# Performance work log

Hardware: AMD Instinct MI355X
Metric: run time of the kernel (lower is better)

The kernel has to match this reference:

```python
import jax, jax.numpy as jnp
import numpy as np

N = 20000      # nodes per snapshot
E = 160000     # edges per snapshot
T = 8          # timesteps
F_IN = 256     # nfeat
HEADS = 4      # GAT heads
C = 128        # nhid_graph (per-head GAT out, concat=False -> mean)
GH = 128       # nhid_gru
NC = 2         # nclass
NEG_SLOPE = 0.2


def setup_inputs() -> dict:
    key = jax.random.key(0)
    ks = jax.random.split(key, 16)
    s = 0.05
    return {
        "graph": jax.random.randint(ks[0], (T, 2, E), 0, N),
        "fts": jax.random.normal(ks[1], (T, N, F_IN), dtype=jnp.float32),
        "time_steps": T,
        # GATConv params (PyG-style): lin weight, att_src/att_dst, bias
        "W_gat": jax.random.normal(ks[2], (F_IN, HEADS * C), dtype=jnp.float32) * s,
        "att_src": jax.random.normal(ks[3], (HEADS, C), dtype=jnp.float32) * s,
        "att_dst": jax.random.normal(ks[4], (HEADS, C), dtype=jnp.float32) * s,
        "b_gat": jax.random.normal(ks[5], (C,), dtype=jnp.float32) * s,
        # GRU params (torch layout: [3H, in], gates order r,z,n)
        "W_ih": jax.random.normal(ks[6], (3 * GH, C), dtype=jnp.float32) * s,
        "W_hh": jax.random.normal(ks[7], (3 * GH, GH), dtype=jnp.float32) * s,
        "b_ih": jax.random.normal(ks[8], (3 * GH,), dtype=jnp.float32) * s,
        "b_hh": jax.random.normal(ks[9], (3 * GH,), dtype=jnp.float32) * s,
        # Attention ('general'): linear_in [H,H] no bias, linear_out [H,2H] no bias
        "W_att_in": jax.random.normal(ks[10], (GH, GH), dtype=jnp.float32) * s,
        "W_att_out": jax.random.normal(ks[11], (GH, 2 * GH), dtype=jnp.float32) * s,
        # final classifier
        "W_cls": jax.random.normal(ks[12], (NC, GH), dtype=jnp.float32) * s,
        "b_cls": jax.random.normal(ks[13], (NC,), dtype=jnp.float32) * s,
    }


def _segment_softmax(logits, seg, num_segments):
    # logits: [E', H], seg: [E'] destination node ids
    m = jax.ops.segment_max(logits, seg, num_segments=num_segments)
    m = jnp.where(jnp.isfinite(m), m, 0.0)
    e = jnp.exp(logits - m[seg])
    s = jax.ops.segment_sum(e, seg, num_segments=num_segments)
    return e / (s[seg] + 1e-16)


def _gat_step(x, edge_index, W_gat, att_src, att_dst, b_gat):
    # PyG GATConv: concat=False (mean over heads), negative_slope=0.2,
    # add_self_loops=True; eval mode so attention dropout is identity.
    n = x.shape[0]
    xw = (x @ W_gat).reshape(n, HEADS, C)                 # [N,H,C]
    loops = jnp.arange(n, dtype=edge_index.dtype)
    src = jnp.concatenate([edge_index[0], loops])         # [E']
    dst = jnp.concatenate([edge_index[1], loops])
    a_src = jnp.einsum('nhc,hc->nh', xw, att_src)         # [N,H]
    a_dst = jnp.einsum('nhc,hc->nh', xw, att_dst)
    alpha = jax.nn.leaky_relu(a_src[src] + a_dst[dst], NEG_SLOPE)  # [E',H]
    alpha = _segment_softmax(alpha, dst, n)
    msg = xw[src] * alpha[..., None]                      # [E',H,C]
    out = jax.ops.segment_sum(msg, dst, num_segments=n)   # [N,H,C]
    return out.mean(axis=1) + b_gat                       # [N,C]


def _gru(y, W_ih, W_hh, b_ih, b_hh):
    # y: [T, N, C]; torch GRU equations, h0 = 0
    n = y.shape[1]
    def step(h, x):
        gi = x @ W_ih.T + b_ih
        gh = h @ W_hh.T + b_hh
        i_r, i_z, i_n = jnp.split(gi, 3, axis=-1)
        h_r, h_z, h_n = jnp.split(gh, 3, axis=-1)
        r = jax.nn.sigmoid(i_r + h_r)
        z = jax.nn.sigmoid(i_z + h_z)
        nn_ = jnp.tanh(i_n + r * h_n)
        h_new = (1.0 - z) * nn_ + z * h
        return h_new, h_new
    h0 = jnp.zeros((n, GH), dtype=y.dtype)
    last, full = jax.lax.scan(step, h0, y)
    return full, last  # [T,N,GH], [N,GH]


def reference(graph, fts, time_steps, W_gat, att_src, att_dst, b_gat,
              W_ih, W_hh, b_ih, b_hh, W_att_in, W_att_out, W_cls, b_cls):
    # per-timestep GAT + leaky_relu(0.2)
    ys = [jax.nn.leaky_relu(
            _gat_step(fts[i], graph[i], W_gat, att_src, att_dst, b_gat),
            NEG_SLOPE)
          for i in range(time_steps)]
    y = jnp.stack(ys)                                     # [T,N,C]
    context, last = _gru(y, W_ih, W_hh, b_ih, b_hh)
    query = last[:, None, :]                              # [N,1,GH]
    context = jnp.transpose(context, (1, 0, 2))           # [N,T,GH]
    # Attention('general')
    q = query @ W_att_in.T                                # [N,1,GH]
    scores = jnp.einsum('nod,ntd->not', q, context)       # [N,1,T]
    w = jax.nn.softmax(scores, axis=-1)
    mix = jnp.einsum('not,ntd->nod', w, context)          # [N,1,GH]
    combined = jnp.concatenate([mix, q], axis=-1)         # [N,1,2GH]
    att_out = jnp.tanh(combined @ W_att_out.T)            # [N,1,GH]
    output = jax.nn.leaky_relu(att_out.reshape(-1, GH), NEG_SLOPE)
    logits = output @ W_cls.T + b_cls                     # [N,NC]
    return jax.nn.log_softmax(logits, axis=1)
```

## Files before the change

### kernel.cpp

```cpp
#include <hip/hip_runtime.h>
#include <hip/hip_bf16.h>
#include <math.h>

#define N_NODES 20000
#define N_EDGES 160000
#define T_STEPS 8
#define F_INC   256
#define HEADS   4
#define CCH     128
#define KC      512
#define GHD     128
#define G3      384
#define SLOPE   0.2f
#define SEG     (N_EDGES + N_NODES)

typedef unsigned short u16;
typedef __attribute__((ext_vector_type(8))) short bf16x8;
typedef __attribute__((ext_vector_type(4))) float f32x4;

__device__ __forceinline__ float leakyf(float x) { return x > 0.f ? x : SLOPE * x; }
__device__ __forceinline__ float b2f(u16 u) {
  union { unsigned int i; float f; } x; x.i = ((unsigned int)u) << 16; return x.f;
}
__device__ __forceinline__ u16 f2b(float f) {
  union { float f; unsigned int i; } u; u.f = f;
  unsigned int r = u.i + 0x7FFFu + ((u.i >> 16) & 1u);
  return (u16)(r >> 16);
}
__device__ __forceinline__ float sigf(float x) { return 1.f / (1.f + expf(-x)); }

__device__ __forceinline__ void gload16(const void* g, void* l) {
  __builtin_amdgcn_global_load_lds(
      (const __attribute__((address_space(1))) unsigned int*)g,
      (__attribute__((address_space(3))) unsigned int*)l, 16, 0, 0);
}

__device__ __forceinline__ bf16x8 cvt8(f32x4 lo, f32x4 hi) {
  union { unsigned int u[4]; bf16x8 v; } r;
  asm("v_cvt_pk_bf16_f32 %0, %1, %2" : "=v"(r.u[0]) : "v"(lo[0]), "v"(lo[1]));
  asm("v_cvt_pk_bf16_f32 %0, %1, %2" : "=v"(r.u[1]) : "v"(lo[2]), "v"(lo[3]));
  asm("v_cvt_pk_bf16_f32 %0, %1, %2" : "=v"(r.u[2]) : "v"(hi[0]), "v"(hi[1]));
  asm("v_cvt_pk_bf16_f32 %0, %1, %2" : "=v"(r.u[3]) : "v"(hi[2]), "v"(hi[3]));
  return r.v;
}

template <int OBF, int FUSE, int AFP32>
__global__ __launch_bounds__(256) void gemm_bf16(
    const void* __restrict__ Ain, const u16* __restrict__ B,
    const float* __restrict__ bias, void* __restrict__ Cout,
    int M, int K, int Nt, int swz,
    const float* __restrict__ attS, const float* __restrict__ attD,
    float* __restrict__ asrc, float* __restrict__ adst)
{
  __shared__ __align__(16) char AsRaw[128 * 32 * 4];
  __shared__ u16 Bs[128][32];
  __shared__ float s_as[128], s_ad[128];
  float* AsF = (float*)AsRaw;
  u16 (*Asb)[32] = (u16(*)[32])AsRaw;
  const int tid  = threadIdx.x;
  const int wave = tid >> 6, lane = tid & 63;
  const int wr = (wave >> 1) * 64, wc = (wave & 1) * 64;
  int bx = blockIdx.x, by = blockIdx.y;
  if (swz) {
    const int gx = gridDim.x;
    const int nwg = gx * (int)gridDim.y;
    const int lin = by * gx + bx;
    const int q = nwg >> 3, r = nwg & 7;
    const int xcd = lin & 7, idx = lin >> 3;
    const int wg = (xcd < r ? xcd * (q + 1) : r * (q + 1) + (xcd - r) * q) + idx;
    bx = wg % gx; by = wg / gx;
  }
  const int bm = by * 128, bn = bx * 128;
  const int l15 = lane & 15, g = lane >> 4;

  if (FUSE && tid < 128) { s_as[tid] = 0.f; s_ad[tid] = 0.f; }

  const int sr = tid >> 2, sd = tid & 3;
  const int ss = sd ^ ((sr >> 1) & 3);
  const u16* aS0 = 0; const u16* aS1 = 0; u16* lA0 = 0; u16* lA1 = 0;
  const float* aF[4]; float* lAF[4];
  if (AFP32) {
    const float* Af = (const float*)Ain;
    const int row0 = tid >> 3, sd8 = tid & 7;
    const int ss8 = sd8 ^ (row0 & 7);
    #pragma unroll
    for (int p = 0; p < 4; ++p) {
      int row = row0 + p * 32;
      aF[p] = Af + (size_t)min(bm + row, M - 1) * K + ss8 * 4;
      lAF[p] = AsF + (size_t)(p * 256 + (tid & ~63)) * 4;
    }
  } else {
    const u16* Ab = (const u16*)Ain;
    aS0 = Ab + (size_t)min(bm + sr,      M - 1) * K + ss * 8;
    aS1 = Ab + (size_t)min(bm + 64 + sr, M - 1) * K + ss * 8;
    lA0 = (u16*)AsRaw + (size_t)(tid & ~63) * 8;
    lA1 = lA0 + 2048;
  }
  const u16* bS0 = B + (size_t)(bn + sr)      * K + ss * 8;
  const u16* bS1 = B + (size_t)(bn + 64 + sr) * K + ss * 8;
  u16* lB0 = &Bs[0][0] + (size_t)(tid & ~63) * 8;
  u16* lB1 = lB0 + 2048;

  f32x4 acc[4][4];
  #pragma unroll
  for (int m = 0; m < 4; ++m)
    #pragma unroll
    for (int n = 0; n < 4; ++n)
      #pragma unroll
      for (int j = 0; j < 4; ++j) acc[m][n][j] = 0.f;

  const int nK = K >> 5;
  for (int kt = 0; kt < nK; ++kt) {
    const int ko = kt * 32;
    if (AFP32) {
      #pragma unroll
      for (int p = 0; p < 4; ++p) gload16(aF[p] + ko, lAF[p]);
    } else {
      gload16(aS0 + ko, lA0);
      gload16(aS1 + ko, lA1);
    }
    gload16(bS0 + ko, lB0);
    gload16(bS1 + ko, lB1);
    __syncthreads();
    bf16x8 af[4], bfr[4];
    #pragma unroll
    for (int m = 0; m < 4; ++m) {
      int row = wr + m * 16 + l15;
      if (AFP32) {
        int s0 = (2 * g) ^ (row & 7), s1 = (2 * g + 1) ^ (row & 7);
        f32x4 lo = *(const f32x4*)&AsF[row * 32 + s0 * 4];
        f32x4 hi = *(const f32x4*)&AsF[row * 32 + s1 * 4];
        af[m] = cvt8(lo, hi);
      } else {
        af[m] = *(const bf16x8*)&Asb[row][(g ^ ((row >> 1) & 3)) * 8];
      }
      int rowb = wc + m * 16 + l15;
      bfr[m] = *(const bf16x8*)&Bs[rowb][(g ^ ((rowb >> 1) & 3)) * 8];
    }
    #pragma unroll
    for (int m = 0; m < 4; ++m)
      #pragma unroll
      for (int n = 0; n < 4; ++n)
        acc[m][n] = __builtin_amdgcn_mfma_f32_16x16x32_bf16(af[m], bfr[n], acc[m][n], 0, 0, 0);
    __syncthreads();
  }
  #pragma unroll
  for (int m = 0; m < 4; ++m) {
    int row0 = bm + wr + m * 16 + g * 4;
    #pragma unroll
    for (int n = 0; n < 4; ++n) {
      int col = bn + wc + n * 16 + l15;
      float bv = bias ? bias[col] : 0.f;
      #pragma unroll
      for (int j = 0; j < 4; ++j) {
        int row = row0 + j;
        if (row < M) {
          float v = acc[m][n][j] + bv;
          if (OBF) ((u16*)Cout)[(size_t)row * Nt + col] = f2b(v);
          else     ((float*)Cout)[(size_t)row * Nt + col] = v;
        }
      }
    }
  }
  if (FUSE) {
    float ps[4][4], pd[4][4];
    #pragma unroll
    for (int m = 0; m < 4; ++m)
      #pragma unroll
      for (int j = 0; j < 4; ++j) { ps[m][j] = 0.f; pd[m][j] = 0.f; }
    #pragma unroll
    for (int n = 0; n < 4; ++n) {
      int cl = wc + n * 16 + l15;
      float wsv = attS[bn + cl], wdv = attD[bn + cl];
      #pragma unroll
      for (int m = 0; m < 4; ++m)
        #pragma unroll
        for (int j = 0; j < 4; ++j) {
          ps[m][j] = fmaf(acc[m][n][j], wsv, ps[m][j]);
          pd[m][j] = fmaf(acc[m][n][j], wdv, pd[m][j]);
        }
    }
    #pragma unroll
    for (int m = 0; m < 4; ++m)
      #pragma unroll
      for (int j = 0; j < 4; ++j)
        #pragma unroll
        for (int msk = 8; msk >= 1; msk >>= 1) {
          ps[m][j] += __shfl_xor(ps[m][j], msk);
          pd[m][j] += __shfl_xor(pd[m][j], msk);
        }
    if (l15 == 0) {
      #pragma unroll
      for (int m = 0; m < 4; ++m)
        #pragma unroll
        for (int j = 0; j < 4; ++j) {
          atomicAdd(&s_as[wr + m * 16 + g * 4 + j], ps[m][j]);
          atomicAdd(&s_ad[wr + m * 16 + g * 4 + j], pd[m][j]);
        }
    }
    __syncthreads();
    if (tid < 128) {
      int row = bm + tid;
      if (row < M) {
        int h = bn >> 7;
        asrc[(size_t)row * 4 + h] = s_as[tid];
        adst[(size_t)row * 4 + h] = s_ad[tid];
      }
    }
  }
}

__global__ void convert_weights(const float* __restrict__ w_ih, const float* __restrict__ w_hh,
                                const float* __restrict__ w_in, const float* __restrict__ w_out,
                                u16* __restrict__ wihb, u16* __restrict__ whhb,
                                u16* __restrict__ winb, u16* __restrict__ woutb)
{
  int i = blockIdx.x * 256 + threadIdx.x;
  const float* src; u16* dst; int base;
  if      (i < 6144)  { src = w_ih;  dst = wihb;  base = i; }
  else if (i < 12288) { src = w_hh;  dst = whhb;  base = i - 6144; }
  else if (i < 14336) { src = w_in;  dst = winb;  base = i - 12288; }
  else                { src = w_out; dst = woutb; base = i - 14336; }
  int o = base * 8;
  float4 v0 = *(const float4*)(src + o);
  float4 v1 = *(const float4*)(src + o + 4);
  bf16x8 ov;
  ov[0] = (short)f2b(v0.x); ov[1] = (short)f2b(v0.y);
  ov[2] = (short)f2b(v0.z); ov[3] = (short)f2b(v0.w);
  ov[4] = (short)f2b(v1.x); ov[5] = (short)f2b(v1.y);
  ov[6] = (short)f2b(v1.z); ov[7] = (short)f2b(v1.w);
  *(bf16x8*)(dst + o) = ov;
}

__global__ void conv_transpose_wgat(const float* __restrict__ src, u16* __restrict__ dst) {
  int idx = blockIdx.x * 256 + threadIdx.x;
  if (idx >= KC * F_INC) return;
  int n = idx >> 8, k = idx & 255;
  dst[(size_t)n * F_INC + k] = f2b(src[(size_t)k * KC + n]);
}

__global__ void count_kernel(const int* __restrict__ graph, int* __restrict__ counts) {
  int e = blockIdx.x * 256 + threadIdx.x;
  int t = blockIdx.y;
  if (e < N_EDGES) {
    int d = graph[(size_t)t * 2 * N_EDGES + N_EDGES + e];
    atomicAdd(&counts[t * N_NODES + d], 1);
  }
}

__global__ __launch_bounds__(1024) void scan_kernel(
    const int* __restrict__ counts, int* __restrict__ offs)
{
  const int t = blockIdx.x;
  const int tid = threadIdx.x, lane = tid & 63, w = tid >> 6;
  __shared__ int s_wt[16];
  int carry = 0;
  const int base_abs = t * SEG;
  for (int base = 0; base < N_NODES; base += 1024) {
    int i = base + tid;
    int v = (i < N_NODES) ? (counts[t * N_NODES + i] + 1) : 0;
    int x = v;
    #pragma unroll
    for (int d = 1; d < 64; d <<= 1) {
      int nvl = __shfl_up(x, d, 64);
      if (lane >= d) x += nvl;
    }
    if (lane == 63) s_wt[w] = x;
    __syncthreads();
    if (tid < 16) {
      int y = s_wt[tid];
      #pragma unroll
      for (int d = 1; d < 16; d <<= 1) {
        int nvl = __shfl_up(y, d, 64);
        if (tid >= d) y += nvl;
      }
      s_wt[tid] = y;
    }
    __syncthreads();
    int wbase = (w > 0) ? s_wt[w - 1] : 0;
    int total = s_wt[15];
    if (i < N_NODES) offs[t * (N_NODES + 1) + i] = base_abs + carry + wbase + x - v;
    carry += total;
    __syncthreads();
  }
  if (tid == 0) offs[t * (N_NODES + 1) + N_NODES] = base_abs + carry;
}

__global__ void scatter_kernel(const int* __restrict__ graph, const int* __restrict__ offs,
                               int* __restrict__ cursor, int* __restrict__ ssrc)
{
  int i = blockIdx.x * 256 + threadIdx.x;
  int t = blockIdx.y;
  if (i >= SEG) return;
  int s, d;
  if (i < N_EDGES) {
    s = graph[(size_t)t * 2 * N_EDGES + i];
    d = graph[(size_t)t * 2 * N_EDGES + N_EDGES + i];
  } else {
    s = d = i - N_EDGES;
  }
  int pos = offs[t * (N_NODES + 1) + d] + atomicAdd(&cursor[t * N_NODES + d], 1);
  ssrc[pos] = s;
}

__global__ __launch_bounds__(256) void aggregate_kernel(
    const u16* __restrict__ xw, const float* __restrict__ a_src,
    const float* __restrict__ a_dst, const float* __restrict__ b_gat,
    const int* __restrict__ offs, const int* __restrict__ ssrc,
    u16* __restrict__ yout)
{
  const int wv = threadIdx.x >> 6, lane = threadIdx.x & 63;
  const int nd = blockIdx.x * 4 + wv;
  const int t  = blockIdx.y;
  const int ob = t * (N_NODES + 1) + nd;
  const int beg = offs[ob], end = offs[ob + 1];
  const size_t rowbase = (size_t)t * N_NODES;
  const int he   = lane & 3;
  const int eidx = lane >> 2;
  const int hl   = lane >> 4;
  const float advh = a_dst[(rowbase + nd) * 4 + he];

  float m = -INFINITY, ssum = 0.f;
  float acc[8] = {0.f,0.f,0.f,0.f,0.f,0.f,0.f,0.f};

#define FMA8(W, X)                                                        \
    { float _w = (W);                                                     \
      acc[0] = fmaf(_w, __uint_as_float((unsigned)(X).x << 16), acc[0]);  \
      acc[1] = fmaf(_w, __uint_as_float((unsigned)(X).x & 0xffff0000u), acc[1]); \
      acc[2] = fmaf(_w, __uint_as_float((unsigned)(X).y << 16), acc[2]);  \
      acc[3] = fmaf(_w, __uint_as_float((unsigned)(X).y & 0xffff0000u), acc[3]); \
      acc[4] = fmaf(_w, __uint_as_float((unsigned)(X).z << 16), acc[4]);  \
      acc[5] = fmaf(_w, __uint_as_float((unsigned)(X).z & 0xffff0000u), acc[5]); \
      acc[6] = fmaf(_w, __uint_as_float((unsigned)(X).w << 16), acc[6]);  \
      acc[7] = fmaf(_w, __uint_as_float((unsigned)(X).w & 0xffff0000u), acc[7]); }
#define LDE(SVAR) (*(const int4*)&xw[(rowbase + (SVAR)) * KC + lane * 8])

  for (int base = beg; base < end; base += 16) {
    const int cnt = min(16, end - base);
    const int e = base + eidx;
    const int sidx = (e < end) ? ssrc[e] : ssrc[base];
    const float av = a_src[(rowbase + sidx) * 4 + he];
    const float a = (eidx < cnt) ? leakyf(av + advh) : -INFINITY;
    float cm = a;
    cm = fmaxf(cm, __shfl_xor(cm, 4));
    cm = fmaxf(cm, __shfl_xor(cm, 8));
    cm = fmaxf(cm, __shfl_xor(cm, 16));
    cm = fmaxf(cm, __shfl_xor(cm, 32));
    const float nm = fmaxf(m, cm);
    const float sc = expf(m - nm);
    const float w = expf(a - nm);
    float ts = w;
    ts += __shfl_xor(ts, 4);
    ts += __shfl_xor(ts, 8);
    ts += __shfl_xor(ts, 16);
    ts += __shfl_xor(ts, 32);
    ssum = ssum * sc + ts;
    m = nm;
    const float schl = __shfl(sc, hl);
    #pragma unroll
    for (int k = 0; k < 8; ++k) acc[k] *= schl;

    const int cpad = (cnt + 3) & ~3;
    int b4 = 0;
    for (; b4 + 8 <= cpad; b4 += 8) {
      const int s0 = __shfl(sidx, (b4 + 0) << 2);
      const int s1 = __shfl(sidx, (b4 + 1) << 2);
      const int s2 = __shfl(sidx, (b4 + 2) << 2);
      const int s3 = __shfl(sidx, (b4 + 3) << 2);
      const int s4 = __shfl(sidx, (b4 + 4) << 2);
      const int s5 = __shfl(sidx, (b4 + 5) << 2);
      const int s6 = __shfl(sidx, (b4 + 6) << 2);
      const int s7 = __shfl(sidx, (b4 + 7) << 2);
      const int4 x0 = LDE(s0); const int4 x1 = LDE(s1);
      const int4 x2 = LDE(s2); const int4 x3 = LDE(s3);
      const int4 x4 = LDE(s4); const int4 x5 = LDE(s5);
      const int4 x6 = LDE(s6); const int4 x7 = LDE(s7);
      const float w0 = __shfl(w, ((b4 + 0) << 2) + hl);
      const float w1 = __shfl(w, ((b4 + 1) << 2) + hl);
      const float w2 = __shfl(w, ((b4 + 2) << 2) + hl);
      const float w3 = __shfl(w, ((b4 + 3) << 2) + hl);
      const float w4 = __shfl(w, ((b4 + 4) << 2) + hl);
      const float w5 = __shfl(w, ((b4 + 5) << 2) + hl);
      const float w6 = __shfl(w, ((b4 + 6) << 2) + hl);
      const float w7 = __shfl(w, ((b4 + 7) << 2) + hl);
      FMA8(w0, x0); FMA8(w1, x1); FMA8(w2, x2); FMA8(w3, x3);
      FMA8(w4, x4); FMA8(w5, x5); FMA8(w6, x6); FMA8(w7, x7);
    }
    if (b4 < cpad) {
      const int s0 = __shfl(sidx, (b4 + 0) << 2);
      const int s1 = __shfl(sidx, (b4 + 1) << 2);
      const int s2 = __shfl(sidx, (b4 + 2) << 2);
      const int s3 = __shfl(sidx, (b4 + 3) << 2);
      const int4 x0 = LDE(s0); const int4 x1 = LDE(s1);
      const int4 x2 = LDE(s2); const int4 x3 = LDE(s3);
      const float w0 = __shfl(w, ((b4 + 0) << 2) + hl);
      const float w1 = __shfl(w, ((b4 + 1) << 2) + hl);
      const float w2 = __shfl(w, ((b4 + 2) << 2) + hl);
      const float w3 = __shfl(w, ((b4 + 3) << 2) + hl);
      FMA8(w0, x0); FMA8(w1, x1); FMA8(w2, x2); FMA8(w3, x3);
    }
  }
#undef LDE
#undef FMA8

  const float sh = __shfl(ssum, hl);
  const float inv = 1.f / (sh + 1e-16f);
  #pragma unroll
  for (int k = 0; k < 8; ++k) {
    acc[k] *= inv;
    acc[k] += __shfl_xor(acc[k], 16);
    acc[k] += __shfl_xor(acc[k], 32);
  }
  if (lane < 16) {
    bf16x8 ov;
    #pragma unroll
    for (int k = 0; k < 8; ++k) {
      float v = acc[k] * 0.25f + b_gat[lane * 8 + k];
      ov[k] = (short)f2b(leakyf(v));
    }
    *(bf16x8*)&yout[(rowbase + nd) * GHD + lane * 8] = ov;
  }
}

__global__ __launch_bounds__(256) void gru_seq(
    const u16* __restrict__ Whh, const float* __restrict__ b_hh,
    const u16* __restrict__ giall, u16* __restrict__ ctx)
{
  __shared__ u16 hA[32][128];
  __shared__ u16 reg2[12288];
  u16 (*Bs)[32] = (u16(*)[32])reg2;
  const int tid = threadIdx.x, lane = tid & 63, wv = tid >> 6;
  const int l15 = lane & 15, g = lane >> 4;
  const int bm = blockIdx.x * 32;

  const int sr = tid >> 2, sd = tid & 3;
  const int ssb = sd ^ ((sr >> 1) & 3);
  const u16* bS[6]; u16* lB[6];
  #pragma unroll
  for (int p = 0; p < 6; ++p) {
    bS[p] = Whh + (size_t)(sr + p * 64) * GHD + ssb * 8;
    lB[p] = reg2 + (size_t)(p * 256 + (tid & ~63)) * 8;
  }
  float bbv[6];
  #pragma unroll
  for (int n = 0; n < 6; ++n) bbv[n] = b_hh[wv * 96 + n * 16 + l15];

  const int cr = tid >> 3;
  const int cg = (tid & 7) * 8;
  const int grow = bm + cr;
  const size_t gb = (size_t)grow * G3;
  const size_t cb = (size_t)grow * GHD;
  float hp[2][8];

  #pragma unroll
  for (int q = 0; q < 2; ++q) {
    const int c0 = cg + q * 64;
    bf16x8 ir8 = *(const bf16x8*)&giall[gb + c0];
    bf16x8 iz8 = *(const bf16x8*)&giall[gb + 128 + c0];
    bf16x8 in8 = *(const bf16x8*)&giall[gb + 256 + c0];
    float4 br0 = *(const float4*)&b_hh[c0];       float4 br1 = *(const float4*)&b_hh[c0 + 4];
    float4 bz0 = *(const float4*)&b_hh[128 + c0]; float4 bz1 = *(const float4*)&b_hh[128 + c0 + 4];
    float4 bn0 = *(const float4*)&b_hh[256 + c0]; float4 bn1 = *(const float4*)&b_hh[256 + c0 + 4];
    float bhr[8] = {br0.x, br0.y, br0.z, br0.w, br1.x, br1.y, br1.z, br1.w};
    float bhz[8] = {bz0.x, bz0.y, bz0.z, bz0.w, bz1.x, bz1.y, bz1.z, bz1.w};
    float bhn[8] = {bn0.x, bn0.y, bn0.z, bn0.w, bn1.x, bn1.y, bn1.z, bn1.w};
    bf16x8 hv;
    #pragma unroll
    for (int k = 0; k < 8; ++k) {
      float rr = sigf(b2f((u16)ir8[k]) + bhr[k]);
      float zz = sigf(b2f((u16)iz8[k]) + bhz[k]);
      float nn = tanhf(b2f((u16)in8[k]) + rr * bhn[k]);
      float h = (1.f - zz) * nn;
      hp[q][k] = h;
      hv[k] = (short)f2b(h);
    }
    const int sl = (c0 >> 3) ^ (cr & 7);
    *(bf16x8*)&hA[cr][sl * 8] = hv;
    *(bf16x8*)&ctx[cb + c0] = hv;
  }
  __syncthreads();

  for (int t = 1; t < T_STEPS; ++t) {
    const u16* gi_t = giall + (size_t)t * N_NODES * G3;
    u16* ctx_t = ctx + (size_t)t * N_NODES * GHD;
    f32x4 acc[2][6];
    #pragma unroll
    for (int m = 0; m < 2; ++m)
      #pragma unroll
      for (int n = 0; n < 6; ++n)
        #pragma unroll
        for (int j = 0; j < 4; ++j) acc[m][n][j] = 0.f;

    #pragma unroll
    for (int kt = 0; kt < 4; ++kt) {
      const int ko = kt * 32;
      #pragma unroll
      for (int p = 0; p < 6; ++p) gload16(bS[p] + ko, lB[p]);
      __syncthreads();
      bf16x8 af[2], bfr[6];
      #pragma unroll
      for (int m = 0; m < 2; ++m) {
        int row = m * 16 + l15;
        int sl = (kt * 4 + g) ^ (row & 7);
        af[m] = *(const bf16x8*)&hA[row][sl * 8];
      }
      #pragma unroll
      for (int n = 0; n < 6; ++n) {
        int rowb = wv * 96 + n * 16 + l15;
        bfr[n] = *(const bf16x8*)&Bs[rowb][(g ^ ((rowb >> 1) & 3)) * 8];
      }
      #pragma unroll
      for (int m = 0; m < 2; ++m)
        #pragma unroll
        for (int n = 0; n < 6; ++n)
          acc[m][n] = __builtin_amdgcn_mfma_f32_16x16x32_bf16(af[m], bfr[n], acc[m][n], 0, 0, 0);
      __syncthreads();
    }
    #pragma unroll
    for (int m = 0; m < 2; ++m)
      #pragma unroll
      for (int n = 0; n < 6; ++n) {
        int c = wv * 96 + n * 16 + l15;
        #pragma unroll
        for (int j = 0; j < 4; ++j) {
          int r = m * 16 + g * 4 + j;
          reg2[r * 384 + (((c >> 3) ^ (r & 7)) << 3) + (c & 7)] = f2b(acc[m][n][j] + bbv[n]);
        }
      }
    __syncthreads();
    #pragma unroll
    for (int q = 0; q < 2; ++q) {
      const int c0 = cg + q * 64;
      const int sl0 = ((c0 >> 3) ^ (cr & 7));
      const int sl1 = (((128 + c0) >> 3) ^ (cr & 7));
      const int sl2 = (((256 + c0) >> 3) ^ (cr & 7));
      bf16x8 hr8 = *(bf16x8*)&reg2[cr * 384 + sl0 * 8];
      bf16x8 hz8 = *(bf16x8*)&reg2[cr * 384 + sl1 * 8];
      bf16x8 hn8 = *(bf16x8*)&reg2[cr * 384 + sl2 * 8];
      bf16x8 ir8 = *(const bf16x8*)&gi_t[gb + c0];
      bf16x8 iz8 = *(const bf16x8*)&gi_t[gb + 128 + c0];
      bf16x8 in8 = *(const bf16x8*)&gi_t[gb + 256 + c0];
      bf16x8 hv;
      #pragma unroll
      for (int k = 0; k < 8; ++k) {
        float rr = sigf(b2f((u16)ir8[k]) + b2f((u16)hr8[k]));
        float zz = sigf(b2f((u16)iz8[k]) + b2f((u16)hz8[k]));
        float nn = tanhf(b2f((u16)in8[k]) + rr * b2f((u16)hn8[k]));
        float h = (1.f - zz) * nn + zz * hp[q][k];
        hp[q][k] = h;
        hv[k] = (short)f2b(h);
      }
      const int slh = (c0 >> 3) ^ (cr & 7);
      *(bf16x8*)&hA[cr][slh * 8] = hv;
      *(bf16x8*)&ctx_t[cb + c0] = hv;
    }
    __syncthreads();
  }
}

__global__ __launch_bounds__(256) void attn_mid(
    const u16* __restrict__ ctx, const float* __restrict__ q,
    u16* __restrict__ comb)
{
  const int node = blockIdx.x * 4 + (threadIdx.x >> 6);
  const int lane = threadIdx.x & 63;
  if (node >= N_NODES) return;
  const float q0 = q[(size_t)node * GHD + lane];
  const float q1 = q[(size_t)node * GHD + 64 + lane];
  float c0[T_STEPS], c1[T_STEPS], w[T_STEPS];
  float mx = -1e30f;
  #pragma unroll
  for (int t = 0; t < T_STEPS; ++t) {
    const u16* cr = ctx + ((size_t)t * N_NODES + node) * GHD;
    c0[t] = b2f(cr[lane]); c1[t] = b2f(cr[64 + lane]);
    float p = q0 * c0[t] + q1 * c1[t];
    #pragma unroll
    for (int m = 32; m >= 1; m >>= 1) p += __shfl_xor(p, m);
    w[t] = p;
    mx = fmaxf(mx, p);
  }
  float s = 0.f;
  #pragma unroll
  for (int t = 0; t < T_STEPS; ++t) { w[t] = expf(w[t] - mx); s += w[t]; }
  const float inv = 1.f / s;
  float m0 = 0.f, m1 = 0.f;
  #pragma unroll
  for (int t = 0; t < T_STEPS; ++t) { m0 = fmaf(w[t], c0[t], m0); m1 = fmaf(w[t], c1[t], m1); }
  m0 *= inv; m1 *= inv;
  u16* cb = comb + (size_t)node * 2 * GHD;
  cb[lane]       = f2b(m0);
  cb[64 + lane]  = f2b(m1);
  cb[128 + lane] = f2b(q0);
  cb[192 + lane] = f2b(q1);
}

__global__ __launch_bounds__(256) void logits_kernel(
    const u16* __restrict__ ao, const float* __restrict__ W_cls,
    const float* __restrict__ b_cls, float* __restrict__ out)
{
  const int node = blockIdx.x * 4 + (threadIdx.x >> 6);
  const int lane = threadIdx.x & 63;
  if (node >= N_NODES) return;
  float o0 = leakyf(tanhf(b2f(ao[(size_t)node * GHD + lane])));
  float o1 = leakyf(tanhf(b2f(ao[(size_t)node * GHD + 64 + lane])));
  float p0 = o0 * W_cls[lane] + o1 * W_cls[64 + lane];
  float p1 = o0 * W_cls[128 + lane] + o1 * W_cls[192 + lane];
  #pragma unroll
  for (int m = 32; m >= 1; m >>= 1) { p0 += __shfl_xor(p0, m); p1 += __shfl_xor(p1, m); }
  if (lane == 0) {
    float l0 = p0 + b_cls[0];
    float l1 = p1 + b_cls[1];
    float mx = fmaxf(l0, l1);
    float lse = mx + logf(expf(l0 - mx) + expf(l1 - mx));
    out[(size_t)node * 2 + 0] = l0 - lse;
    out[(size_t)node * 2 + 1] = l1 - lse;
  }
}

extern "C" void kernel_launch(void* const* d_in, const int* in_sizes, int n_in,
                              void* d_out, int out_size, void* d_ws, size_t ws_size,
                              hipStream_t stream)
{
  const int*   graph     = (const int*)  d_in[0];
  const float* fts       = (const float*)d_in[1];
  const float* W_gat     = (const float*)d_in[3];
  const float* att_src   = (const float*)d_in[4];
  const float* att_dst   = (const float*)d_in[5];
  const float* b_gat     = (const float*)d_in[6];
  const float* W_ih      = (const float*)d_in[7];
  const float* W_hh      = (const float*)d_in[8];
  const float* b_ih      = (const float*)d_in[9];
  const float* b_hh      = (const float*)d_in[10];
  const float* W_att_in  = (const float*)d_in[11];
  const float* W_att_out = (const float*)d_in[12];
  const float* W_cls     = (const float*)d_in[13];
  const float* b_cls     = (const float*)d_in[14];
  float* out = (float*)d_out;

  char* ws = (char*)d_ws;
  size_t off = 0;
  auto alloc = [&](size_t bytes) {
    void* p = ws + off;
    off = (off + bytes + 255) & ~(size_t)255;
    return p;
  };
  const size_t NT = (size_t)T_STEPS * N_NODES;
  u16*   wgatT = (u16*)alloc((size_t)KC * F_INC * 2);
  u16*   wihb  = (u16*)alloc((size_t)G3 * GHD * 2);
  u16*   whhb  = (u16*)alloc((size_t)G3 * GHD * 2);
  u16*   winb  = (u16*)alloc((size_t)GHD * GHD * 2);
  u16*   woutb = (u16*)alloc((size_t)GHD * 2 * GHD * 2);
  u16*   xw    = (u16*)alloc(NT * KC * 2);
  float* asrc  = (float*)alloc(NT * 4 * 4);
  float* adst  = (float*)alloc(NT * 4 * 4);
  u16*   yall  = (u16*)alloc(NT * GHD * 2);
  u16*   giall = (u16*)alloc(NT * G3 * 2);
  u16*   ctx   = (u16*)alloc(NT * GHD * 2);
  float* qf    = (float*)alloc((size_t)N_NODES * GHD * 4);
  u16*   comb  = (u16*)alloc((size_t)N_NODES * 2 * GHD * 2);
  u16*   aob   = (u16*)alloc((size_t)N_NODES * GHD * 2);
  int* counts  = (int*)alloc((size_t)2 * T_STEPS * N_NODES * 4);
  int* cursor  = counts + T_STEPS * N_NODES;
  int* offs    = (int*)alloc((size_t)T_STEPS * (N_NODES + 1) * 4);
  int* ssrc    = (int*)alloc((size_t)T_STEPS * SEG * 4);

  conv_transpose_wgat<<<dim3((KC * F_INC + 255) / 256), 256, 0, stream>>>(W_gat, wgatT);
  convert_weights<<<dim3(72), 256, 0, stream>>>(W_ih, W_hh, W_att_in, W_att_out,
                                                wihb, whhb, winb, woutb);

  hipMemsetAsync(counts, 0, (size_t)2 * T_STEPS * N_NODES * 4, stream);
  count_kernel<<<dim3(N_EDGES / 256, T_STEPS), 256, 0, stream>>>(graph, counts);
  scan_kernel<<<dim3(T_STEPS), 1024, 0, stream>>>(counts, offs);
  scatter_kernel<<<dim3((SEG + 255) / 256, T_STEPS), 256, 0, stream>>>(graph, offs, cursor, ssrc);

  gemm_bf16<1, 1, 1><<<dim3(KC / 128, (int)(NT / 128)), 256, 0, stream>>>(
      fts, wgatT, nullptr, xw, (int)NT, F_INC, KC, 1, att_src, att_dst, asrc, adst);

  aggregate_kernel<<<dim3(N_NODES / 4, T_STEPS), 256, 0, stream>>>(
      xw, asrc, adst, b_gat, offs, ssrc, yall);

  gemm_bf16<1, 0, 0><<<dim3(G3 / 128, (int)(NT / 128)), 256, 0, stream>>>(
      yall, wihb, b_ih, giall, (int)NT, GHD, G3, 1, nullptr, nullptr, nullptr, nullptr);

  gru_seq<<<dim3(N_NODES / 32), 256, 0, stream>>>(whhb, b_hh, giall, ctx);

  gemm_bf16<0, 0, 0><<<dim3(1, (N_NODES + 127) / 128), 256, 0, stream>>>(
      ctx + (size_t)(T_STEPS - 1) * N_NODES * GHD, winb, nullptr, qf,
      N_NODES, GHD, GHD, 0, nullptr, nullptr, nullptr, nullptr);
  attn_mid<<<dim3(N_NODES / 4), 256, 0, stream>>>(ctx, qf, comb);
  gemm_bf16<1, 0, 0><<<dim3(1, (N_NODES + 127) / 128), 256, 0, stream>>>(
      comb, woutb, nullptr, aob, N_NODES, 2 * GHD, GHD, 0, nullptr, nullptr, nullptr, nullptr);
  logits_kernel<<<dim3(N_NODES / 4), 256, 0, stream>>>(aob, W_cls, b_cls, out);
}
```

Baseline: 744.4 us.

## Fuse input GEMM into GRU, fuse classifier into output GEMM, parallelize scan

```diff
diff --git a/kernel.cpp b/kernel.cpp
--- a/kernel.cpp
+++ b/kernel.cpp
@@ -13,6 +13,8 @@
 #define G3      384
 #define SLOPE   0.2f
 #define SEG     (N_EDGES + N_NODES)
+#define TN      (T_STEPS * N_NODES)
+#define SCAN_BLKS ((TN + 1023) / 1024)
 
 typedef unsigned short u16;
 typedef __attribute__((ext_vector_type(8))) short bf16x8;
@@ -144,20 +146,22 @@
         acc[m][n] = __builtin_amdgcn_mfma_f32_16x16x32_bf16(af[m], bfr[n], acc[m][n], 0, 0, 0);
     __syncthreads();
   }
-  #pragma unroll
-  for (int m = 0; m < 4; ++m) {
-    int row0 = bm + wr + m * 16 + g * 4;
-    #pragma unroll
-    for (int n = 0; n < 4; ++n) {
-      int col = bn + wc + n * 16 + l15;
-      float bv = bias ? bias[col] : 0.f;
-      #pragma unroll
-      for (int j = 0; j < 4; ++j) {
-        int row = row0 + j;
-        if (row < M) {
-          float v = acc[m][n][j] + bv;
-          if (OBF) ((u16*)Cout)[(size_t)row * Nt + col] = f2b(v);
-          else     ((float*)Cout)[(size_t)row * Nt + col] = v;
+  if (FUSE != 2) {
+    #pragma unroll
+    for (int m = 0; m < 4; ++m) {
+      int row0 = bm + wr + m * 16 + g * 4;
+      #pragma unroll
+      for (int n = 0; n < 4; ++n) {
+        int col = bn + wc + n * 16 + l15;
+        float bv = bias ? bias[col] : 0.f;
+        #pragma unroll
+        for (int j = 0; j < 4; ++j) {
+          int row = row0 + j;
+          if (row < M) {
+            float v = acc[m][n][j] + bv;
+            if (OBF) ((u16*)Cout)[(size_t)row * Nt + col] = f2b(v);
+            else     ((float*)Cout)[(size_t)row * Nt + col] = v;
+          }
         }
       }
     }
@@ -176,8 +180,10 @@
       for (int m = 0; m < 4; ++m)
         #pragma unroll
         for (int j = 0; j < 4; ++j) {
-          ps[m][j] = fmaf(acc[m][n][j], wsv, ps[m][j]);
-          pd[m][j] = fmaf(acc[m][n][j], wdv, pd[m][j]);
+          float av = acc[m][n][j];
+          if (FUSE == 2) av = leakyf(tanhf(av));
+          ps[m][j] = fmaf(av, wsv, ps[m][j]);
+          pd[m][j] = fmaf(av, wdv, pd[m][j]);
         }
     }
     #pragma unroll
@@ -202,9 +208,18 @@
     if (tid < 128) {
       int row = bm + tid;
       if (row < M) {
-        int h = bn >> 7;
-        asrc[(size_t)row * 4 + h] = s_as[tid];
-        adst[(size_t)row * 4 + h] = s_ad[tid];
+        if (FUSE == 1) {
+          int h = bn >> 7;
+          asrc[(size_t)row * 4 + h] = s_as[tid];
+          adst[(size_t)row * 4 + h] = s_ad[tid];
+        } else {
+          float l0 = s_as[tid] + bias[0];
+          float l1 = s_ad[tid] + bias[1];
+          float mx = fmaxf(l0, l1);
+          float lse = mx + logf(expf(l0 - mx) + expf(l1 - mx));
+          asrc[(size_t)row * 2 + 0] = l0 - lse;
+          asrc[(size_t)row * 2 + 1] = l1 - lse;
+        }
       }
     }
   }
@@ -248,42 +263,57 @@
   }
 }
 
-__global__ __launch_bounds__(1024) void scan_kernel(
-    const int* __restrict__ counts, int* __restrict__ offs)
-{
-  const int t = blockIdx.x;
+__global__ __launch_bounds__(1024) void scanA(
+    const int* __restrict__ counts, int* __restrict__ offs, int* __restrict__ bsums)
+{
   const int tid = threadIdx.x, lane = tid & 63, w = tid >> 6;
   __shared__ int s_wt[16];
+  int i = blockIdx.x * 1024 + tid;
+  int v = (i < TN) ? (counts[i] + 1) : 0;
+  int x = v;
+  #pragma unroll
+  for (int d = 1; d < 64; d <<= 1) {
+    int nvl = __shfl_up(x, d, 64);
+    if (lane >= d) x += nvl;
+  }
+  if (lane == 63) s_wt[w] = x;
+  __syncthreads();
+  if (tid < 16) {
+    int y = s_wt[tid];
+    #pragma unroll
+    for (int d = 1; d < 16; d <<= 1) {
+      int nvl = __shfl_up(y, d, 64);
+      if (tid >= d) y += nvl;
+    }
+    s_wt[tid] = y;
+  }
+  __syncthreads();
+  int wbase = (w > 0) ? s_wt[w - 1] : 0;
+  if (i < TN) offs[i] = wbase + x - v;
+  if (tid == 1023) bsums[blockIdx.x] = s_wt[15];
+}
+
+__global__ void scanB(int* __restrict__ bsums, int* __restrict__ offs) {
+  const int lane = threadIdx.x;
   int carry = 0;
-  const int base_abs = t * SEG;
-  for (int base = 0; base < N_NODES; base += 1024) {
-    int i = base + tid;
-    int v = (i < N_NODES) ? (counts[t * N_NODES + i] + 1) : 0;
+  for (int base = 0; base < 192; base += 64) {
+    int idx = base + lane;
+    int v = (idx < SCAN_BLKS) ? bsums[idx] : 0;
     int x = v;
     #pragma unroll
     for (int d = 1; d < 64; d <<= 1) {
       int nvl = __shfl_up(x, d, 64);
       if (lane >= d) x += nvl;
     }
-    if (lane == 63) s_wt[w] = x;
-    __syncthreads();
-    if (tid < 16) {
-      int y = s_wt[tid];
-      #pragma unroll
-      for (int d = 1; d < 16; d <<= 1) {
-        int nvl = __shfl_up(y, d, 64);
-        if (tid >= d) y += nvl;
-      }
-      s_wt[tid] = y;
-    }
-    __syncthreads();
-    int wbase = (w > 0) ? s_wt[w - 1] : 0;
-    int total = s_wt[15];
-    if (i < N_NODES) offs[t * (N_NODES + 1) + i] = base_abs + carry + wbase + x - v;
-    carry += total;
-    __syncthreads();
-  }
-  if (tid == 0) offs[t * (N_NODES + 1) + N_NODES] = base_abs + carry;
+    if (idx < SCAN_BLKS) bsums[idx] = carry + x - v;
+    carry += __shfl(x, 63);
+  }
+  if (lane == 0) offs[TN] = carry;
+}
+
+__global__ __launch_bounds__(1024) void scanC(int* __restrict__ offs, const int* __restrict__ bsums) {
+  int i = blockIdx.x * 1024 + threadIdx.x;
+  if (i < TN) offs[i] += bsums[blockIdx.x];
 }
 
 __global__ void scatter_kernel(const int* __restrict__ graph, const int* __restrict__ offs,
@@ -299,7 +329,7 @@
   } else {
     s = d = i - N_EDGES;
   }
-  int pos = offs[t * (N_NODES + 1) + d] + atomicAdd(&cursor[t * N_NODES + d], 1);
+  int pos = offs[t * N_NODES + d] + atomicAdd(&cursor[t * N_NODES + d], 1);
   ssrc[pos] = s;
 }
 
@@ -312,7 +342,7 @@
   const int wv = threadIdx.x >> 6, lane = threadIdx.x & 63;
   const int nd = blockIdx.x * 4 + wv;
   const int t  = blockIdx.y;
-  const int ob = t * (N_NODES + 1) + nd;
+  const int ob = t * N_NODES + nd;
   const int beg = offs[ob], end = offs[ob + 1];
   const size_t rowbase = (size_t)t * N_NODES;
   const int he   = lane & 3;
@@ -423,97 +453,93 @@
 }
 
 __global__ __launch_bounds__(256) void gru_seq(
-    const u16* __restrict__ Whh, const float* __restrict__ b_hh,
-    const u16* __restrict__ giall, u16* __restrict__ ctx)
-{
-  __shared__ u16 hA[32][128];
-  __shared__ u16 reg2[12288];
-  u16 (*Bs)[32] = (u16(*)[32])reg2;
+    const u16* __restrict__ Whh, const u16* __restrict__ Wih,
+    const float* __restrict__ b_hh, const float* __restrict__ b_ih,
+    const u16* __restrict__ yall, u16* __restrict__ ctx)
+{
+  __shared__ u16 hA[32 * 128];
+  __shared__ u16 yA[32 * 128];
+  __shared__ u16 w1[384 * 32];
+  __shared__ u16 w2[384 * 32];
   const int tid = threadIdx.x, lane = tid & 63, wv = tid >> 6;
   const int l15 = lane & 15, g = lane >> 4;
   const int bm = blockIdx.x * 32;
 
   const int sr = tid >> 2, sd = tid & 3;
   const int ssb = sd ^ ((sr >> 1) & 3);
-  const u16* bS[6]; u16* lB[6];
+  const u16* hS[6]; const u16* iS[6]; u16* l1p[6]; u16* l2p[6];
   #pragma unroll
   for (int p = 0; p < 6; ++p) {
-    bS[p] = Whh + (size_t)(sr + p * 64) * GHD + ssb * 8;
-    lB[p] = reg2 + (size_t)(p * 256 + (tid & ~63)) * 8;
-  }
-  float bbv[6];
-  #pragma unroll
-  for (int n = 0; n < 6; ++n) bbv[n] = b_hh[wv * 96 + n * 16 + l15];
-
-  const int cr = tid >> 3;
-  const int cg = (tid & 7) * 8;
-  const int grow = bm + cr;
-  const size_t gb = (size_t)grow * G3;
-  const size_t cb = (size_t)grow * GHD;
+    hS[p] = Whh + (size_t)(sr + p * 64) * GHD + ssb * 8;
+    iS[p] = Wih + (size_t)(sr + p * 64) * GHD + ssb * 8;
+    l1p[p] = w1 + (size_t)(p * 256 + (tid & ~63)) * 8;
+    l2p[p] = w2 + (size_t)(p * 256 + (tid & ~63)) * 8;
+  }
+  const int yr0 = tid >> 4,        ys0 = tid & 15, gs0 = ys0 ^ (yr0 & 7);
+  const int yr1 = (tid + 256) >> 4, gs1 = (tid & 15) ^ (yr1 & 7);
+  u16* yd0 = yA + (size_t)(tid & ~63) * 8;
+  u16* yd1 = yA + (size_t)(256 + (tid & ~63)) * 8;
+  float bbh[6], bbi[6];
+  #pragma unroll
+  for (int n = 0; n < 6; ++n) {
+    bbh[n] = b_hh[wv * 96 + n * 16 + l15];
+    bbi[n] = b_ih[wv * 96 + n * 16 + l15];
+  }
+  const int cr = tid >> 3, cg = (tid & 7) * 8;
+  const size_t cb = (size_t)(bm + cr) * GHD;
   float hp[2][8];
-
-  #pragma unroll
-  for (int q = 0; q < 2; ++q) {
-    const int c0 = cg + q * 64;
-    bf16x8 ir8 = *(const bf16x8*)&giall[gb + c0];
-    bf16x8 iz8 = *(const bf16x8*)&giall[gb + 128 + c0];
-    bf16x8 in8 = *(const bf16x8*)&giall[gb + 256 + c0];
-    float4 br0 = *(const float4*)&b_hh[c0];       float4 br1 = *(const float4*)&b_hh[c0 + 4];
-    float4 bz0 = *(const float4*)&b_hh[128 + c0]; float4 bz1 = *(const float4*)&b_hh[128 + c0 + 4];
-    float4 bn0 = *(const float4*)&b_hh[256 + c0]; float4 bn1 = *(const float4*)&b_hh[256 + c0 + 4];
-    float bhr[8] = {br0.x, br0.y, br0.z, br0.w, br1.x, br1.y, br1.z, br1.w};
-    float bhz[8] = {bz0.x, bz0.y, bz0.z, bz0.w, bz1.x, bz1.y, bz1.z, bz1.w};
-    float bhn[8] = {bn0.x, bn0.y, bn0.z, bn0.w, bn1.x, bn1.y, bn1.z, bn1.w};
-    bf16x8 hv;
-    #pragma unroll
-    for (int k = 0; k < 8; ++k) {
-      float rr = sigf(b2f((u16)ir8[k]) + bhr[k]);
-      float zz = sigf(b2f((u16)iz8[k]) + bhz[k]);
-      float nn = tanhf(b2f((u16)in8[k]) + rr * bhn[k]);
-      float h = (1.f - zz) * nn;
-      hp[q][k] = h;
-      hv[k] = (short)f2b(h);
-    }
-    const int sl = (c0 >> 3) ^ (cr & 7);
-    *(bf16x8*)&hA[cr][sl * 8] = hv;
-    *(bf16x8*)&ctx[cb + c0] = hv;
+  #pragma unroll
+  for (int q = 0; q < 2; ++q)
+    #pragma unroll
+    for (int k = 0; k < 8; ++k) hp[q][k] = 0.f;
+
+  {
+    bf16x8 z8 = {0,0,0,0,0,0,0,0};
+    *(bf16x8*)&hA[tid * 16] = z8;
+    *(bf16x8*)&hA[tid * 16 + 8] = z8;
   }
   __syncthreads();
 
-  for (int t = 1; t < T_STEPS; ++t) {
-    const u16* gi_t = giall + (size_t)t * N_NODES * G3;
-    u16* ctx_t = ctx + (size_t)t * N_NODES * GHD;
-    f32x4 acc[2][6];
+  for (int t = 0; t < T_STEPS; ++t) {
+    const u16* ysrc = yall + ((size_t)t * N_NODES + bm) * GHD;
+    gload16(ysrc + (size_t)yr0 * GHD + gs0 * 8, yd0);
+    gload16(ysrc + (size_t)yr1 * GHD + gs1 * 8, yd1);
+    f32x4 accG[2][6], accI[2][6];
     #pragma unroll
     for (int m = 0; m < 2; ++m)
       #pragma unroll
       for (int n = 0; n < 6; ++n)
         #pragma unroll
-        for (int j = 0; j < 4; ++j) acc[m][n][j] = 0.f;
+        for (int j = 0; j < 4; ++j) { accG[m][n][j] = 0.f; accI[m][n][j] = 0.f; }
 
     #pragma unroll
     for (int kt = 0; kt < 4; ++kt) {
       const int ko = kt * 32;
       #pragma unroll
-      for (int p = 0; p < 6; ++p) gload16(bS[p] + ko, lB[p]);
+      for (int p = 0; p < 6; ++p) { gload16(hS[p] + ko, l1p[p]); gload16(iS[p] + ko, l2p[p]); }
       __syncthreads();
-      bf16x8 af[2], bfr[6];
+      bf16x8 afh[2], afy[2], bh[6], bi[6];
       #pragma unroll
       for (int m = 0; m < 2; ++m) {
         int row = m * 16 + l15;
         int sl = (kt * 4 + g) ^ (row & 7);
-        af[m] = *(const bf16x8*)&hA[row][sl * 8];
+        afh[m] = *(const bf16x8*)&hA[row * 128 + sl * 8];
+        afy[m] = *(const bf16x8*)&yA[row * 128 + sl * 8];
       }
       #pragma unroll
       for (int n = 0; n < 6; ++n) {
         int rowb = wv * 96 + n * 16 + l15;
-        bfr[n] = *(const bf16x8*)&Bs[rowb][(g ^ ((rowb >> 1) & 3)) * 8];
+        int slb = g ^ ((rowb >> 1) & 3);
+        bh[n] = *(const bf16x8*)&w1[rowb * 32 + slb * 8];
+        bi[n] = *(const bf16x8*)&w2[rowb * 32 + slb * 8];
       }
       #pragma unroll
       for (int m = 0; m < 2; ++m)
         #pragma unroll
-        for (int n = 0; n < 6; ++n)
-          acc[m][n] = __builtin_amdgcn_mfma_f32_16x16x32_bf16(af[m], bfr[n], acc[m][n], 0, 0, 0);
+        for (int n = 0; n < 6; ++n) {
+          accG[m][n] = __builtin_amdgcn_mfma_f32_16x16x32_bf16(afh[m], bh[n], accG[m][n], 0, 0, 0);
+          accI[m][n] = __builtin_amdgcn_mfma_f32_16x16x32_bf16(afy[m], bi[n], accI[m][n], 0, 0, 0);
+        }
       __syncthreads();
     }
     #pragma unroll
@@ -524,22 +550,25 @@
         #pragma unroll
         for (int j = 0; j < 4; ++j) {
           int r = m * 16 + g * 4 + j;
-          reg2[r * 384 + (((c >> 3) ^ (r & 7)) << 3) + (c & 7)] = f2b(acc[m][n][j] + bbv[n]);
+          int o = r * 384 + (((c >> 3) ^ (r & 7)) << 3) + (c & 7);
+          w1[o] = f2b(accG[m][n][j] + bbh[n]);
+          w2[o] = f2b(accI[m][n][j] + bbi[n]);
         }
       }
     __syncthreads();
+    u16* ctx_t = ctx + (size_t)t * N_NODES * GHD;
     #pragma unroll
     for (int q = 0; q < 2; ++q) {
       const int c0 = cg + q * 64;
       const int sl0 = ((c0 >> 3) ^ (cr & 7));
       const int sl1 = (((128 + c0) >> 3) ^ (cr & 7));
       const int sl2 = (((256 + c0) >> 3) ^ (cr & 7));
-      bf16x8 hr8 = *(bf16x8*)&reg2[cr * 384 + sl0 * 8];
-      bf16x8 hz8 = *(bf16x8*)&reg2[cr * 384 + sl1 * 8];
-      bf16x8 hn8 = *(bf16x8*)&reg2[cr * 384 + sl2 * 8];
-      bf16x8 ir8 = *(const bf16x8*)&gi_t[gb + c0];
-      bf16x8 iz8 = *(const bf16x8*)&gi_t[gb + 128 + c0];
-      bf16x8 in8 = *(const bf16x8*)&gi_t[gb + 256 + c0];
+      bf16x8 hr8 = *(bf16x8*)&w1[cr * 384 + sl0 * 8];
+      bf16x8 hz8 = *(bf16x8*)&w1[cr * 384 + sl1 * 8];
+      bf16x8 hn8 = *(bf16x8*)&w1[cr * 384 + sl2 * 8];
+      bf16x8 ir8 = *(bf16x8*)&w2[cr * 384 + sl0 * 8];
+      bf16x8 iz8 = *(bf16x8*)&w2[cr * 384 + sl1 * 8];
+      bf16x8 in8 = *(bf16x8*)&w2[cr * 384 + sl2 * 8];
       bf16x8 hv;
       #pragma unroll
       for (int k = 0; k < 8; ++k) {
@@ -550,8 +579,7 @@
         hp[q][k] = h;
         hv[k] = (short)f2b(h);
       }
-      const int slh = (c0 >> 3) ^ (cr & 7);
-      *(bf16x8*)&hA[cr][slh * 8] = hv;
+      *(bf16x8*)&hA[cr * 128 + ((c0 >> 3) ^ (cr & 7)) * 8] = hv;
       *(bf16x8*)&ctx_t[cb + c0] = hv;
     }
     __syncthreads();
@@ -592,29 +620,6 @@
   cb[64 + lane]  = f2b(m1);
   cb[128 + lane] = f2b(q0);
   cb[192 + lane] = f2b(q1);
-}
-
-__global__ __launch_bounds__(256) void logits_kernel(
-    const u16* __restrict__ ao, const float* __restrict__ W_cls,
-    const float* __restrict__ b_cls, float* __restrict__ out)
-{
-  const int node = blockIdx.x * 4 + (threadIdx.x >> 6);
-  const int lane = threadIdx.x & 63;
-  if (node >= N_NODES) return;
-  float o0 = leakyf(tanhf(b2f(ao[(size_t)node * GHD + lane])));
-  float o1 = leakyf(tanhf(b2f(ao[(size_t)node * GHD + 64 + lane])));
-  float p0 = o0 * W_cls[lane] + o1 * W_cls[64 + lane];
-  float p1 = o0 * W_cls[128 + lane] + o1 * W_cls[192 + lane];
-  #pragma unroll
-  for (int m = 32; m >= 1; m >>= 1) { p0 += __shfl_xor(p0, m); p1 += __shfl_xor(p1, m); }
-  if (lane == 0) {
-    float l0 = p0 + b_cls[0];
-    float l1 = p1 + b_cls[1];
-    float mx = fmaxf(l0, l1);
-    float lse = mx + logf(expf(l0 - mx) + expf(l1 - mx));
-    out[(size_t)node * 2 + 0] = l0 - lse;
-    out[(size_t)node * 2 + 1] = l1 - lse;
-  }
 }
 
 extern "C" void kernel_launch(void* const* d_in, const int* in_sizes, int n_in,
@@ -644,7 +649,7 @@
     off = (off + bytes + 255) & ~(size_t)255;
     return p;
   };
-  const size_t NT = (size_t)T_STEPS * N_NODES;
+  const size_t NT = (size_t)TN;
   u16*   wgatT = (u16*)alloc((size_t)KC * F_INC * 2);
   u16*   wihb  = (u16*)alloc((size_t)G3 * GHD * 2);
   u16*   whhb  = (u16*)alloc((size_t)G3 * GHD * 2);
@@ -654,23 +659,24 @@
   float* asrc  = (float*)alloc(NT * 4 * 4);
   float* adst  = (float*)alloc(NT * 4 * 4);
   u16*   yall  = (u16*)alloc(NT * GHD * 2);
-  u16*   giall = (u16*)alloc(NT * G3 * 2);
   u16*   ctx   = (u16*)alloc(NT * GHD * 2);
   float* qf    = (float*)alloc((size_t)N_NODES * GHD * 4);
   u16*   comb  = (u16*)alloc((size_t)N_NODES * 2 * GHD * 2);
-  u16*   aob   = (u16*)alloc((size_t)N_NODES * GHD * 2);
-  int* counts  = (int*)alloc((size_t)2 * T_STEPS * N_NODES * 4);
-  int* cursor  = counts + T_STEPS * N_NODES;
-  int* offs    = (int*)alloc((size_t)T_STEPS * (N_NODES + 1) * 4);
+  int* counts  = (int*)alloc((size_t)2 * TN * 4);
+  int* cursor  = counts + TN;
+  int* offs    = (int*)alloc((size_t)(TN + 1) * 4);
+  int* bsums   = (int*)alloc((size_t)256 * 4);
   int* ssrc    = (int*)alloc((size_t)T_STEPS * SEG * 4);
 
   conv_transpose_wgat<<<dim3((KC * F_INC + 255) / 256), 256, 0, stream>>>(W_gat, wgatT);
   convert_weights<<<dim3(72), 256, 0, stream>>>(W_ih, W_hh, W_att_in, W_att_out,
                                                 wihb, whhb, winb, woutb);
 
-  hipMemsetAsync(counts, 0, (size_t)2 * T_STEPS * N_NODES * 4, stream);
+  hipMemsetAsync(counts, 0, (size_t)2 * TN * 4, stream);
   count_kernel<<<dim3(N_EDGES / 256, T_STEPS), 256, 0, stream>>>(graph, counts);
-  scan_kernel<<<dim3(T_STEPS), 1024, 0, stream>>>(counts, offs);
+  scanA<<<dim3(SCAN_BLKS), 1024, 0, stream>>>(counts, offs, bsums);
+  scanB<<<dim3(1), 64, 0, stream>>>(bsums, offs);
+  scanC<<<dim3(SCAN_BLKS), 1024, 0, stream>>>(offs, bsums);
   scatter_kernel<<<dim3((SEG + 255) / 256, T_STEPS), 256, 0, stream>>>(graph, offs, cursor, ssrc);
 
   gemm_bf16<1, 1, 1><<<dim3(KC / 128, (int)(NT / 128)), 256, 0, stream>>>(
@@ -679,16 +685,13 @@
   aggregate_kernel<<<dim3(N_NODES / 4, T_STEPS), 256, 0, stream>>>(
       xw, asrc, adst, b_gat, offs, ssrc, yall);
 
-  gemm_bf16<1, 0, 0><<<dim3(G3 / 128, (int)(NT / 128)), 256, 0, stream>>>(
-      yall, wihb, b_ih, giall, (int)NT, GHD, G3, 1, nullptr, nullptr, nullptr, nullptr);
-
-  gru_seq<<<dim3(N_NODES / 32), 256, 0, stream>>>(whhb, b_hh, giall, ctx);
+  gru_seq<<<dim3(N_NODES / 32), 256, 0, stream>>>(whhb, wihb, b_hh, b_ih, yall, ctx);
 
   gemm_bf16<0, 0, 0><<<dim3(1, (N_NODES + 127) / 128), 256, 0, stream>>>(
       ctx + (size_t)(T_STEPS - 1) * N_NODES * GHD, winb, nullptr, qf,
       N_NODES, GHD, GHD, 0, nullptr, nullptr, nullptr, nullptr);
   attn_mid<<<dim3(N_NODES / 4), 256, 0, stream>>>(ctx, qf, comb);
-  gemm_bf16<1, 0, 0><<<dim3(1, (N_NODES + 127) / 128), 256, 0, stream>>>(
-      comb, woutb, nullptr, aob, N_NODES, 2 * GHD, GHD, 0, nullptr, nullptr, nullptr, nullptr);
-  logits_kernel<<<dim3(N_NODES / 4), 256, 0, stream>>>(aob, W_cls, b_cls, out);
-}
+  gemm_bf16<0, 2, 0><<<dim3(1, (N_NODES + 127) / 128), 256, 0, stream>>>(
+      comb, woutb, b_cls, nullptr, N_NODES, 2 * GHD, GHD, 0,
+      W_cls, W_cls + GHD, out, nullptr);
+}
```

After: 745.5 us. No clear change (+0.2%).
